# Kernel tuning notes

Measured on AMD Instinct MI355X. Metric: run time of the kernel, lower is better.

The kernel has to match this reference:

```python
import jax, jax.numpy as jnp
import numpy as np

B, C, O, N, T, K = 4, 64, 64, 32768, 4, 9
PAD, DIL = 4, 1  # padding*dilation, dilation
SIGMA = 0.05
EPS_BN = 1e-5


def _gather_ch(x, idx):
    # x: [B, C, N], idx: [B, N] -> gather along last dim per channel
    idx3 = jnp.broadcast_to(idx[:, None, :], x.shape)
    return jnp.take_along_axis(x, idx3, axis=-1)


def _weighted_conv(x, coords, w):
    # x: [B,C,N], coords: [B,3,N], w: [O,C,K]
    xp = jnp.pad(x, ((0, 0), (0, 0), (PAD, PAD)))
    cp = jnp.pad(coords, ((0, 0), (0, 0), (PAD, PAD)))
    win_idx = jnp.arange(N)[:, None] + jnp.arange(K) * DIL  # [N, K]
    win = xp[:, :, win_idx]   # [B,C,N,K]
    cwin = cp[:, :, win_idx]  # [B,3,N,K]
    d = cwin - cwin[:, :, :, K // 2:K // 2 + 1]
    s = jnp.sum(d * d, axis=1)                    # [B,N,K]
    r = jnp.sqrt(jnp.where(s > 0, s, 1.0))
    r = jnp.where(s > 0, r, 0.0)
    wgt = jnp.maximum(1.0 - r / SIGMA, 0.0)       # [B,N,K]
    return jnp.einsum('bcnk,bnk,ock->bon', win, wgt, w)


def _bn(x, g, b):
    # training-mode BatchNorm1d over (B, N)
    m = jnp.mean(x, axis=(0, 2), keepdims=True)
    v = jnp.var(x, axis=(0, 2), keepdims=True)
    return g[None, :, None] * (x - m) * jax.lax.rsqrt(v + EPS_BN) + b[None, :, None]


def setup_inputs() -> dict:
    key = jax.random.key(0)
    ks = jax.random.split(key, 12)
    inp = jax.random.normal(ks[0], (B, C, N), dtype=jnp.float32)
    # coords in a small box so sigma=0.05 yields non-trivial weights
    multi_coords = jax.random.uniform(ks[1], (B, 3, N, T), dtype=jnp.float32) * 0.02
    indices = jax.random.randint(ks[2], (B, N, T), 0, N, dtype=jnp.int32)
    reindices = jax.random.randint(ks[3], (B, N, T), 0, N, dtype=jnp.int32)
    fan = C * K
    conv_w = jax.random.normal(ks[4], (T, O, C, K), dtype=jnp.float32) / np.sqrt(fan)
    bn_gamma = jnp.ones((T, O), dtype=jnp.float32)
    bn_beta = jnp.zeros((T, O), dtype=jnp.float32)
    fusion_w = jax.random.normal(ks[5], (O, T * O), dtype=jnp.float32) / np.sqrt(T * O)
    fusion_b = jnp.zeros((O,), dtype=jnp.float32)
    fusion_gamma = jnp.ones((O,), dtype=jnp.float32)
    fusion_beta = jnp.zeros((O,), dtype=jnp.float32)
    return {"input": inp, "multi_coords": multi_coords, "indices": indices,
            "reindices": reindices, "conv_w": conv_w, "bn_gamma": bn_gamma,
            "bn_beta": bn_beta, "fusion_w": fusion_w, "fusion_b": fusion_b,
            "fusion_gamma": fusion_gamma, "fusion_beta": fusion_beta}


def reference(input, multi_coords, indices, reindices, conv_w, bn_gamma, bn_beta,
              fusion_w, fusion_b, fusion_gamma, fusion_beta):
    outs = []
    for i in range(T):  # fixed small set of 4 Hilbert orders
        x = _gather_ch(input, indices[:, :, i])            # [B,C,N]
        x = _weighted_conv(x, multi_coords[:, :, :, i], conv_w[i])  # [B,O,N]
        x = _bn(x, bn_gamma[i], bn_beta[i])
        x = _gather_ch(x, reindices[:, :, i])
        outs.append(x)
    cat = jnp.concatenate(outs, axis=1)                    # [B, T*O, N]
    y = jnp.einsum('bcn,oc->bon', cat, fusion_w) + fusion_b[None, :, None]
    y = _bn(y, fusion_gamma, fusion_beta)
    return jax.nn.relu(y)
```

## Files before the change

kernel.cpp:

```cpp
#include <hip/hip_runtime.h>
#include <hip/hip_bf16.h>

#define BB 4
#define CC 64
#define OO 64
#define NN 32768
#define TT 4
#define KK 9
#define PADW 4
#define SIGMA 0.05f
#define EPS_BN 1e-5f

typedef __attribute__((ext_vector_type(8))) short bf16x8;
typedef __attribute__((ext_vector_type(4))) float f32x4;

__device__ __forceinline__ unsigned short f2bf(float f) {
  __hip_bfloat16 h = __float2bfloat16(f);
  return *reinterpret_cast<unsigned short*>(&h);
}
__device__ __forceinline__ float bf2f(unsigned short u) {
  unsigned int x = ((unsigned int)u) << 16;
  float f;
  __builtin_memcpy(&f, &x, 4);
  return f;
}
__device__ __forceinline__ unsigned int pkbf(float a, float b) {
  float2 t; t.x = a; t.y = b;
  __hip_bfloat162 h = __float22bfloat162_rn(t);
  unsigned int r;
  __builtin_memcpy(&r, &h, 4);
  return r;
}

__global__ __launch_bounds__(256) void transpose_kernel(
    const float* __restrict__ inp, unsigned short* __restrict__ xTb)
{
  const int n0 = blockIdx.x * 64;
  const int b  = blockIdx.y;
  const int tid = threadIdx.x;
  __shared__ float xt[64][65];
  {
    int nl = tid & 63, c4 = tid >> 6;
    #pragma unroll
    for (int i = 0; i < 16; ++i) {
      int c = c4 * 16 + i;
      xt[c][nl] = inp[((size_t)(b*CC + c))*NN + n0 + nl];
    }
  }
  __syncthreads();
  {
    int nl = tid >> 2, cq = tid & 3;
    unsigned int pk[8];
    #pragma unroll
    for (int i = 0; i < 8; ++i) {
      int c = cq*16 + i*2;
      pk[i] = pkbf(xt[c][nl], xt[c+1][nl]);
    }
    unsigned int* dst = (unsigned int*)(xTb + (((size_t)b*NN) + n0 + nl)*CC + cq*16);
    ((int4*)dst)[0] = make_int4((int)pk[0],(int)pk[1],(int)pk[2],(int)pk[3]);
    ((int4*)dst)[1] = make_int4((int)pk[4],(int)pk[5],(int)pk[6],(int)pk[7]);
  }
}

__global__ __launch_bounds__(256) void wprep_kernel(
    const float* __restrict__ cw, unsigned short* __restrict__ W4)
{
  const int k = blockIdx.x;
  const int t = blockIdx.y;
  for (int u = threadIdx.x; u < OO*CC; u += 256) {
    int o = u >> 6, c = u & 63;
    int ow = o >> 5, ot = (o >> 4) & 1, l15 = o & 15;
    int frag = c >> 5, q = (c >> 3) & 3, j = c & 7;
    float wv = cw[(((size_t)(t*OO + o))*CC + c)*KK + k];
    W4[(size_t)(t*9+k)*4096 + ow*2048 + ot*1024 + frag*512 + l15*32 + q*8 + j]
        = f2bf(wv);
  }
}

__global__ __launch_bounds__(256, 4) void conv_kernel(
    const unsigned short* __restrict__ xTb,
    const float* __restrict__ mc,
    const int*   __restrict__ ind,
    const unsigned short* __restrict__ W4,
    unsigned short* __restrict__ Y,
    float* __restrict__ cpart2)
{
  const int n0  = blockIdx.x * 128;
  const int b   = blockIdx.y;
  const int t   = blockIdx.z;
  const int tid = threadIdx.x;
  const int lane = tid & 63;
  const int w    = tid >> 6;
  const int l15  = lane & 15;
  const int q    = lane >> 4;
  const int ow   = w & 1;
  const int nw   = w >> 1;

  __shared__ short xg[136][72];
  __shared__ float wgl[128][10];
  __shared__ float mcs[3][140];

  int4 g[5];
  #pragma unroll
  for (int i = 0; i < 5; ++i) {
    int u = tid + 256*i;
    g[i] = make_int4(0,0,0,0);
    if (u < 1088) {
      int p = u >> 3, s = u & 7;
      int m = n0 + p - PADW;
      if (m >= 0 && m < NN) {
        int idx = ind[((size_t)b*NN + m)*TT + t];
        g[i] = *(const int4*)(xTb + ((size_t)b*NN + idx)*CC + s*8);
      }
    }
  }

  if (tid < 136) {
    int m = n0 + tid - PADW;
    #pragma unroll
    for (int d = 0; d < 3; ++d) {
      float4 v = make_float4(0.f, 0.f, 0.f, 0.f);
      if (m >= 0 && m < NN)
        v = *(const float4*)(mc + (((size_t)(b*3+d))*NN + m)*TT);
      mcs[d][tid] = (t==0) ? v.x : (t==1) ? v.y : (t==2) ? v.z : v.w;
    }
  }

  #pragma unroll
  for (int i = 0; i < 5; ++i) {
    int u = tid + 256*i;
    if (u < 1088) {
      int p = u >> 3, s = u & 7;
      *(int4*)&xg[p][s*8] = g[i];
    }
  }
  __syncthreads();

  {
    int nl = tid >> 1;
    int k0 = (tid & 1) * 5;
    int kc = 5 - (tid & 1);
    float cx = mcs[0][nl+4], cy = mcs[1][nl+4], cz = mcs[2][nl+4];
    for (int i2 = 0; i2 < kc; ++i2) {
      int k = k0 + i2, mi = nl + k;
      float dx = mcs[0][mi]-cx, dy = mcs[1][mi]-cy, dz = mcs[2][mi]-cz;
      float s2 = dx*dx + dy*dy + dz*dz;
      float r = (s2 > 0.f) ? sqrtf(s2) : 0.f;
      wgl[nl][k] = fmaxf(1.f - r*(1.f/SIGMA), 0.f);
    }
  }
  __syncthreads();

  const unsigned short* Wt = W4 + (size_t)t*9*4096 + ow*2048 + (l15*4 + q)*8;
  const f32x4 Z = {0.f, 0.f, 0.f, 0.f};
  f32x4 fin[2][4];
  #pragma unroll
  for (int ot = 0; ot < 2; ++ot)
    #pragma unroll
    for (int ns = 0; ns < 4; ++ns) fin[ot][ns] = Z;

  for (int k = 0; k < KK; ++k) {
    const unsigned short* Wk = Wt + (size_t)k*4096;
    bf16x8 af[2][2];
    #pragma unroll
    for (int ot = 0; ot < 2; ++ot) {
      af[ot][0] = *(const bf16x8*)(Wk + ot*1024);
      af[ot][1] = *(const bf16x8*)(Wk + ot*1024 + 512);
    }
    #pragma unroll
    for (int ns = 0; ns < 4; ++ns) {
      int nl = nw*64 + ns*16 + l15;
      int p  = nl + k;
      bf16x8 b0 = *(const bf16x8*)&xg[p][q*8];
      bf16x8 b1 = *(const bf16x8*)&xg[p][32 + q*8];
      float wgt = wgl[nl][k];
      #pragma unroll
      for (int ot = 0; ot < 2; ++ot) {
        f32x4 d = __builtin_amdgcn_mfma_f32_16x16x32_bf16(af[ot][0], b0, Z, 0, 0, 0);
        d = __builtin_amdgcn_mfma_f32_16x16x32_bf16(af[ot][1], b1, d, 0, 0, 0);
        fin[ot][ns] += wgt * d;
      }
    }
  }

  #pragma unroll
  for (int ns = 0; ns < 4; ++ns) {
    int nl = nw*64 + ns*16 + l15;
    size_t row = (((size_t)t*BB + b)*NN + n0 + nl)*OO;
    #pragma unroll
    for (int ot = 0; ot < 2; ++ot) {
      uint2 pk2;
      pk2.x = pkbf(fin[ot][ns][0], fin[ot][ns][1]);
      pk2.y = pkbf(fin[ot][ns][2], fin[ot][ns][3]);
      *(uint2*)(Y + row + ow*32 + ot*16 + q*4) = pk2;
    }
  }

  float sv[16];
  #pragma unroll
  for (int ot = 0; ot < 2; ++ot)
    #pragma unroll
    for (int r = 0; r < 4; ++r) {
      float a = 0.f, qs = 0.f;
      #pragma unroll
      for (int ns = 0; ns < 4; ++ns) {
        float v = fin[ot][ns][r];
        a += v; qs += v*v;
      }
      sv[ot*4+r] = a; sv[8+ot*4+r] = qs;
    }
  #pragma unroll
  for (int msk = 1; msk < 16; msk <<= 1) {
    #pragma unroll
    for (int i = 0; i < 16; ++i) sv[i] += __shfl_xor(sv[i], msk, 16);
  }
  if (l15 == 0) {
    int slot4 = ((b*256 + (int)blockIdx.x) << 2) | w;
    #pragma unroll
    for (int ot = 0; ot < 2; ++ot)
      #pragma unroll
      for (int r = 0; r < 4; ++r) {
        int o = ow*32 + ot*16 + q*4 + r;
        cpart2[((size_t)((t*64 + o)*2 + 0))*4096 + slot4] = sv[ot*4+r];
        cpart2[((size_t)((t*64 + o)*2 + 1))*4096 + slot4] = sv[8+ot*4+r];
      }
  }
}

__global__ __launch_bounds__(256) void bnparam_kernel(
    const float* __restrict__ cpart2,
    const float* __restrict__ gam,
    const float* __restrict__ bet,
    float* __restrict__ ss)
{
  const int to = blockIdx.x;
  const int tid = threadIdx.x;
  __shared__ float r1[256], r2[256];
  const float* p1 = cpart2 + (size_t)to*2*4096;
  const float* p2 = p1 + 4096;
  float s1 = 0.f, s2 = 0.f;
  for (int i = tid*4; i < 4096; i += 1024) {
    float4 a = *(const float4*)(p1 + i);
    float4 c = *(const float4*)(p2 + i);
    s1 += a.x + a.y + a.z + a.w;
    s2 += c.x + c.y + c.z + c.w;
  }
  r1[tid] = s1; r2[tid] = s2;
  __syncthreads();
  for (int st = 128; st > 0; st >>= 1) {
    if (tid < st) { r1[tid] += r1[tid+st]; r2[tid] += r2[tid+st]; }
    __syncthreads();
  }
  if (tid == 0) {
    const float inv = 1.f / (float)(BB * NN);
    float mean = r1[0] * inv;
    float var  = r2[0] * inv - mean * mean;
    float sc = gam[to] * rsqrtf(var + EPS_BN);
    ss[to*2 + 0] = sc;
    ss[to*2 + 1] = bet[to] - mean * sc;
  }
}

__global__ __launch_bounds__(256, 4) void fusion_kernel(
    const unsigned short* __restrict__ Y,
    const int*   __restrict__ rind,
    const float* __restrict__ ss,
    const float* __restrict__ fw,
    const float* __restrict__ fb,
    float* __restrict__ out)
{
  const int n0  = blockIdx.x * 128;
  const int b   = blockIdx.y;
  const int tid = threadIdx.x;
  const int lane = tid & 63;
  const int w    = tid >> 6;
  const int l15  = lane & 15;
  const int q    = lane >> 4;
  const int ow   = w & 1;
  const int nw   = w >> 1;

  __shared__ short zg[128][72];
  __shared__ int   rnl[TT][128];
  __shared__ float ssl[512];

  for (int u = tid; u < 512; u += 256) {
    int tt = u >> 7, nl = u & 127;
    rnl[tt][nl] = rind[((size_t)b*NN + n0 + nl)*TT + tt];
  }
  ssl[tid]       = ss[tid];
  ssl[tid + 256] = ss[tid + 256];
  __syncthreads();

  f32x4 fin[2][4];
  #pragma unroll
  for (int ot = 0; ot < 2; ++ot)
    #pragma unroll
    for (int ns = 0; ns < 4; ++ns) fin[ot][ns] = (f32x4){0.f,0.f,0.f,0.f};

  for (int r = 0; r < 4; ++r) {
    if (r) __syncthreads();
    #pragma unroll
    for (int i = 0; i < 4; ++i) {
      int u = tid + 256*i;
      int n = u >> 3, s = u & 7;
      int rn = rnl[r][n];
      int4 raw = *(const int4*)(Y + (((size_t)r*BB + b)*NN + rn)*OO + s*8);
      const unsigned short* rp = (const unsigned short*)&raw;
      int cb = r*64 + s*8;
      unsigned int pk[4];
      #pragma unroll
      for (int j = 0; j < 4; ++j) {
        float v0 = bf2f(rp[2*j  ]) * ssl[(cb+2*j  )*2] + ssl[(cb+2*j  )*2+1];
        float v1 = bf2f(rp[2*j+1]) * ssl[(cb+2*j+1)*2] + ssl[(cb+2*j+1)*2+1];
        pk[j] = pkbf(v0, v1);
      }
      *(int4*)&zg[n][s*8] = make_int4((int)pk[0],(int)pk[1],(int)pk[2],(int)pk[3]);
    }
    __syncthreads();

    #pragma unroll
    for (int kk = 0; kk < 2; ++kk) {
      bf16x8 af[2];
      #pragma unroll
      for (int ot = 0; ot < 2; ++ot) {
        const float* wp = fw + (size_t)(ow*32 + ot*16 + l15)*256 + r*64 + kk*32 + q*8;
        float4 wa = *(const float4*)wp;
        float4 wb = *(const float4*)(wp + 4);
        unsigned int u0 = pkbf(wa.x, wa.y), u1 = pkbf(wa.z, wa.w);
        unsigned int u2 = pkbf(wb.x, wb.y), u3 = pkbf(wb.z, wb.w);
        int4 tmp = make_int4((int)u0,(int)u1,(int)u2,(int)u3);
        __builtin_memcpy(&af[ot], &tmp, 16);
      }
      #pragma unroll
      for (int ns = 0; ns < 4; ++ns) {
        int nl = nw*64 + ns*16 + l15;
        bf16x8 bfr = *(const bf16x8*)&zg[nl][kk*32 + q*8];
        #pragma unroll
        for (int ot = 0; ot < 2; ++ot)
          fin[ot][ns] = __builtin_amdgcn_mfma_f32_16x16x32_bf16(af[ot], bfr, fin[ot][ns], 0, 0, 0);
      }
    }
  }

  #pragma unroll
  for (int ot = 0; ot < 2; ++ot)
    #pragma unroll
    for (int rr = 0; rr < 4; ++rr) {
      int o = ow*32 + ot*16 + q*4 + rr;
      float bias = fb[o];
      float* dst = out + ((size_t)(b*OO + o))*NN + n0 + nw*64;
      #pragma unroll
      for (int ns = 0; ns < 4; ++ns)
        dst[ns*16 + l15] = fin[ot][ns][rr] + bias;
    }
}

__global__ __launch_bounds__(256) void fstat_kernel(
    const float* __restrict__ out, float* __restrict__ fpart)
{
  const int o = blockIdx.x, b = blockIdx.y;
  const int tid = threadIdx.x;
  __shared__ float r1[256], r2[256];
  const float* src = out + ((size_t)(b*OO + o))*NN;
  float s1 = 0.f, s2 = 0.f;
  for (int i = tid*4; i < NN; i += 1024) {
    float4 v = *(const float4*)(src + i);
    s1 += v.x + v.y + v.z + v.w;
    s2 += v.x*v.x + v.y*v.y + v.z*v.z + v.w*v.w;
  }
  r1[tid] = s1; r2[tid] = s2;
  __syncthreads();
  for (int st = 128; st > 0; st >>= 1) {
    if (tid < st) { r1[tid] += r1[tid+st]; r2[tid] += r2[tid+st]; }
    __syncthreads();
  }
  if (tid == 0) {
    fpart[(b*OO + o)*2 + 0] = r1[0];
    fpart[(b*OO + o)*2 + 1] = r2[0];
  }
}

__global__ void freduce_kernel(
    const float* __restrict__ fpart,
    const float* __restrict__ fg,
    const float* __restrict__ fbeta,
    float* __restrict__ fss)
{
  int o = threadIdx.x;
  float s1 = 0.f, s2 = 0.f;
  #pragma unroll
  for (int b = 0; b < BB; ++b) {
    s1 += fpart[(b*OO + o)*2 + 0];
    s2 += fpart[(b*OO + o)*2 + 1];
  }
  const float inv = 1.f / (float)(BB * NN);
  float mean = s1 * inv;
  float var  = s2 * inv - mean * mean;
  float sc = fg[o] * rsqrtf(var + EPS_BN);
  fss[o*2 + 0] = sc;
  fss[o*2 + 1] = fbeta[o] - mean * sc;
}

__global__ __launch_bounds__(256) void final_kernel(
    float* __restrict__ out, const float* __restrict__ fss)
{
  const int e0 = blockIdx.x * 2048 + threadIdx.x;
  #pragma unroll
  for (int s = 0; s < 8; ++s) {
    int e  = e0 + s * 256;
    int o2 = (e >> 15) & 63;
    float sc = fss[o2*2 + 0];
    float sh = fss[o2*2 + 1];
    float v = out[e] * sc + sh;
    out[e] = fmaxf(v, 0.f);
  }
}

extern "C" void kernel_launch(void* const* d_in, const int* in_sizes, int n_in,
                              void* d_out, int out_size, void* d_ws, size_t ws_size,
                              hipStream_t stream) {
  const float* inp  = (const float*)d_in[0];
  const float* mc   = (const float*)d_in[1];
  const int*   ind  = (const int*)  d_in[2];
  const int*   rind = (const int*)  d_in[3];
  const float* cw   = (const float*)d_in[4];
  const float* bg   = (const float*)d_in[5];
  const float* bb   = (const float*)d_in[6];
  const float* fw   = (const float*)d_in[7];
  const float* fb   = (const float*)d_in[8];
  const float* fg   = (const float*)d_in[9];
  const float* fbt  = (const float*)d_in[10];

  char* ws = (char*)d_ws;
  float* convss = (float*)(ws + 0);
  float* fss    = (float*)(ws + 2048);
  float* fpart  = (float*)(ws + 2560);
  unsigned short* Y = (unsigned short*)(ws + 8192);

  char* ob = (char*)d_out;
  unsigned short* xTb = (unsigned short*)ob;
  unsigned short* W4  = (unsigned short*)(ob + 16777216);
  float*          cpart2 = (float*)(ob + 17072128);
  float* out = (float*)d_out;

  dim3 gt(NN/64, BB);
  transpose_kernel<<<gt, 256, 0, stream>>>(inp, xTb);

  dim3 gw(KK, TT);
  wprep_kernel<<<gw, 256, 0, stream>>>(cw, W4);

  dim3 gc(NN/128, BB, TT);
  conv_kernel<<<gc, 256, 0, stream>>>(xTb, mc, ind, W4, Y, cpart2);

  bnparam_kernel<<<256, 256, 0, stream>>>(cpart2, bg, bb, convss);

  dim3 gf(NN/128, BB);
  fusion_kernel<<<gf, 256, 0, stream>>>(Y, rind, convss, fw, fb, out);

  dim3 gs(OO, BB);
  fstat_kernel<<<gs, 256, 0, stream>>>(out, fpart);

  freduce_kernel<<<1, 64, 0, stream>>>(fpart, fg, fbt, fss);

  final_kernel<<<(BB*OO*NN)/2048, 256, 0, stream>>>(out, fss);
}
```

Baseline: 238.3 us.

## Fold conv BN affine into fusion weights and bias, read gathered Y directly

Folds the per-channel BN scale of each conv branch into the fusion weights and the BN shift into a precomputed fusion bias (a new tiny kernel). The fusion kernel then feeds the gathered bf16 Y rows straight into MFMA from global memory, dropping the LDS staging buffer, its per-element affine transform and the syncs. It also vectorizes the final BN+ReLU pass with float4 accesses. In exchange it adds one small kernel launch, and the gathered rows are read without the coalesced LDS stage, so rows are fetched directly per MFMA fragment. Rounding changes slightly because the scale is applied to the weights before the bf16 cast.

```diff
diff --git a/kernel.cpp b/kernel.cpp
--- a/kernel.cpp
+++ b/kernel.cpp
@@ -261,12 +261,22 @@
   }
 }
 
-__global__ __launch_bounds__(256, 4) void fusion_kernel(
+__global__ void bias2_kernel(
+    const float* __restrict__ fw, const float* __restrict__ ss,
+    const float* __restrict__ fb, float* __restrict__ bias2)
+{
+  int o = threadIdx.x;
+  float s = fb[o];
+  for (int c = 0; c < 256; ++c) s += fw[o*256 + c] * ss[c*2 + 1];
+  bias2[o] = s;
+}
+
+__global__ __launch_bounds__(256) void fusion_kernel(
     const unsigned short* __restrict__ Y,
     const int*   __restrict__ rind,
     const float* __restrict__ ss,
     const float* __restrict__ fw,
-    const float* __restrict__ fb,
+    const float* __restrict__ bias2,
     float* __restrict__ out)
 {
   const int n0  = blockIdx.x * 128;
@@ -279,16 +289,17 @@
   const int ow   = w & 1;
   const int nw   = w >> 1;
 
-  __shared__ short zg[128][72];
   __shared__ int   rnl[TT][128];
-  __shared__ float ssl[512];
-
-  for (int u = tid; u < 512; u += 256) {
-    int tt = u >> 7, nl = u & 127;
-    rnl[tt][nl] = rind[((size_t)b*NN + n0 + nl)*TT + tt];
-  }
-  ssl[tid]       = ss[tid];
-  ssl[tid + 256] = ss[tid + 256];
+  __shared__ float scl[256];
+  __shared__ float b2l[64];
+
+  if (tid < 128) {
+    int4 r4 = *(const int4*)(rind + ((size_t)b*NN + n0 + tid)*TT);
+    rnl[0][tid] = r4.x; rnl[1][tid] = r4.y;
+    rnl[2][tid] = r4.z; rnl[3][tid] = r4.w;
+  }
+  scl[tid] = ss[tid*2];
+  if (tid < 64) b2l[tid] = bias2[tid];
   __syncthreads();
 
   f32x4 fin[2][4];
@@ -298,46 +309,29 @@
     for (int ns = 0; ns < 4; ++ns) fin[ot][ns] = (f32x4){0.f,0.f,0.f,0.f};
 
   for (int r = 0; r < 4; ++r) {
-    if (r) __syncthreads();
-    #pragma unroll
-    for (int i = 0; i < 4; ++i) {
-      int u = tid + 256*i;
-      int n = u >> 3, s = u & 7;
-      int rn = rnl[r][n];
-      int4 raw = *(const int4*)(Y + (((size_t)r*BB + b)*NN + rn)*OO + s*8);
-      const unsigned short* rp = (const unsigned short*)&raw;
-      int cb = r*64 + s*8;
-      unsigned int pk[4];
-      #pragma unroll
-      for (int j = 0; j < 4; ++j) {
-        float v0 = bf2f(rp[2*j  ]) * ssl[(cb+2*j  )*2] + ssl[(cb+2*j  )*2+1];
-        float v1 = bf2f(rp[2*j+1]) * ssl[(cb+2*j+1)*2] + ssl[(cb+2*j+1)*2+1];
-        pk[j] = pkbf(v0, v1);
-      }
-      *(int4*)&zg[n][s*8] = make_int4((int)pk[0],(int)pk[1],(int)pk[2],(int)pk[3]);
-    }
-    __syncthreads();
-
+    const unsigned short* Yb = Y + ((size_t)r*BB + b)*NN*OO;
     #pragma unroll
     for (int kk = 0; kk < 2; ++kk) {
       bf16x8 af[2];
       #pragma unroll
       for (int ot = 0; ot < 2; ++ot) {
         const float* wp = fw + (size_t)(ow*32 + ot*16 + l15)*256 + r*64 + kk*32 + q*8;
-        float4 wa = *(const float4*)wp;
-        float4 wb = *(const float4*)(wp + 4);
-        unsigned int u0 = pkbf(wa.x, wa.y), u1 = pkbf(wa.z, wa.w);
-        unsigned int u2 = pkbf(wb.x, wb.y), u3 = pkbf(wb.z, wb.w);
-        int4 tmp = make_int4((int)u0,(int)u1,(int)u2,(int)u3);
+        const float* sp = scl + r*64 + kk*32 + q*8;
+        unsigned int pk[4];
+        #pragma unroll
+        for (int j = 0; j < 4; ++j)
+          pk[j] = pkbf(wp[2*j]*sp[2*j], wp[2*j+1]*sp[2*j+1]);
+        int4 tmp = make_int4((int)pk[0],(int)pk[1],(int)pk[2],(int)pk[3]);
         __builtin_memcpy(&af[ot], &tmp, 16);
       }
       #pragma unroll
       for (int ns = 0; ns < 4; ++ns) {
         int nl = nw*64 + ns*16 + l15;
-        bf16x8 bfr = *(const bf16x8*)&zg[nl][kk*32 + q*8];
+        int rn = rnl[r][nl];
+        bf16x8 braw = *(const bf16x8*)(Yb + (size_t)rn*OO + kk*32 + q*8);
         #pragma unroll
         for (int ot = 0; ot < 2; ++ot)
-          fin[ot][ns] = __builtin_amdgcn_mfma_f32_16x16x32_bf16(af[ot], bfr, fin[ot][ns], 0, 0, 0);
+          fin[ot][ns] = __builtin_amdgcn_mfma_f32_16x16x32_bf16(af[ot], braw, fin[ot][ns], 0, 0, 0);
       }
     }
   }
@@ -347,7 +341,7 @@
     #pragma unroll
     for (int rr = 0; rr < 4; ++rr) {
       int o = ow*32 + ot*16 + q*4 + rr;
-      float bias = fb[o];
+      float bias = b2l[o];
       float* dst = out + ((size_t)(b*OO + o))*NN + n0 + nw*64;
       #pragma unroll
       for (int ns = 0; ns < 4; ++ns)
@@ -404,15 +398,19 @@
 __global__ __launch_bounds__(256) void final_kernel(
     float* __restrict__ out, const float* __restrict__ fss)
 {
-  const int e0 = blockIdx.x * 2048 + threadIdx.x;
-  #pragma unroll
-  for (int s = 0; s < 8; ++s) {
-    int e  = e0 + s * 256;
-    int o2 = (e >> 15) & 63;
+  const size_t base = (size_t)blockIdx.x * 2048 + threadIdx.x * 4;
+  #pragma unroll
+  for (int s = 0; s < 2; ++s) {
+    size_t e = base + (size_t)s * 1024;
+    int o2 = (int)((e >> 15) & 63);
     float sc = fss[o2*2 + 0];
     float sh = fss[o2*2 + 1];
-    float v = out[e] * sc + sh;
-    out[e] = fmaxf(v, 0.f);
+    float4 v = *(float4*)(out + e);
+    v.x = fmaxf(v.x*sc + sh, 0.f);
+    v.y = fmaxf(v.y*sc + sh, 0.f);
+    v.z = fmaxf(v.z*sc + sh, 0.f);
+    v.w = fmaxf(v.w*sc + sh, 0.f);
+    *(float4*)(out + e) = v;
   }
 }
 
@@ -435,6 +433,7 @@
   float* convss = (float*)(ws + 0);
   float* fss    = (float*)(ws + 2048);
   float* fpart  = (float*)(ws + 2560);
+  float* bias2  = (float*)(ws + 4608);
   unsigned short* Y = (unsigned short*)(ws + 8192);
 
   char* ob = (char*)d_out;
@@ -454,8 +453,10 @@
 
   bnparam_kernel<<<256, 256, 0, stream>>>(cpart2, bg, bb, convss);
 
+  bias2_kernel<<<1, 64, 0, stream>>>(fw, convss, fb, bias2);
+
   dim3 gf(NN/128, BB);
-  fusion_kernel<<<gf, 256, 0, stream>>>(Y, rind, convss, fw, fb, out);
+  fusion_kernel<<<gf, 256, 0, stream>>>(Y, rind, convss, fw, bias2, out);
 
   dim3 gs(OO, BB);
   fstat_kernel<<<gs, 256, 0, stream>>>(out, fpart);
```

Measured after the change: 254.2 us. +6.7%, slower.
